# Kernel tuning notes

Hardware: AMD Instinct MI355X
Metric: run time of the kernel (lower is better)

Reference implementation:

```python
import jax, jax.numpy as jnp
import numpy as np

P = 2  # lrtd_pad (p_l == p_r == p_t == p_d)
B, C, H, W = 4, 64, 128, 128


def setup_inputs() -> dict:
    key = jax.random.key(0)
    x = jax.random.normal(key, (B, 6, C, H, W), dtype=jnp.float32)
    return {"x": x}


def _cube_pad(x):
    # faces: [B,C,H,W] each; order matches torch module unpacking
    fb, fd, ff, fl, fr, ft = (x[:, i] for i in range(6))
    flip_h = lambda a: a[:, :, ::-1, :]   # flip along dim 2 (rows)
    flip_w = lambda a: a[:, :, :, ::-1]   # flip along dim 3 (cols)
    T = lambda a: jnp.swapaxes(a, 2, 3)   # permute(0,1,3,2)

    # top strips for faces 0..5 -> [B,6,C,P,W]
    top = jnp.stack([
        flip_h(ft[:, :, :P, :]),           # back
        ff[:, :, -P:, :],                  # down
        ft[:, :, -P:, :],                  # front
        T(ft[:, :, :, :P]),                # left
        flip_h(T(ft[:, :, :, -P:])),       # right
        flip_h(fb[:, :, :P, :]),           # top
    ], axis=1)

    # bottom strips -> [B,6,C,P,W]
    bot = jnp.stack([
        flip_h(fd[:, :, -P:, :]),
        flip_h(fb[:, :, -P:, :]),
        fd[:, :, :P, :],
        flip_h(T(fd[:, :, :, :P])),
        T(fd[:, :, :, -P:]),
        ff[:, :, :P, :],
    ], axis=1)

    # left strips -> [B,6,C,H,P]
    lft = jnp.stack([
        fr[:, :, :, -P:],
        flip_w(T(fl[:, :, -P:, :])),
        fl[:, :, :, -P:],
        fb[:, :, :, -P:],
        ff[:, :, :, -P:],
        T(fl[:, :, :P, :]),
    ], axis=1)

    # right strips -> [B,6,C,H,P]
    rgt = jnp.stack([
        fl[:, :, :, :P],
        T(fr[:, :, -P:, :]),
        fr[:, :, :, :P],
        ff[:, :, :, :P],
        fb[:, :, :, :P],
        flip_w(T(fr[:, :, :P, :])),
    ], axis=1)

    # corners: equal pads -> repeat the top/bottom strip's edge column along width
    p_tl = jnp.tile(top[:, :, :, :P, :1], (1, 1, 1, 1, P))
    p_tr = jnp.tile(top[:, :, :, -P:, -1:], (1, 1, 1, 1, P))
    p_dl = jnp.tile(bot[:, :, :, :P, :1], (1, 1, 1, 1, P))
    p_dr = jnp.tile(bot[:, :, :, -P:, -1:], (1, 1, 1, 1, P))

    mid = jnp.concatenate([top, x, bot], axis=3)            # [B,6,C,H+2P,W]
    left = jnp.concatenate([p_tl, lft, p_dl], axis=3)       # [B,6,C,H+2P,P]
    right = jnp.concatenate([p_tr, rgt, p_dr], axis=3)      # [B,6,C,H+2P,P]
    return jnp.concatenate([left, mid, right], axis=4)      # [B,6,C,H+2P,W+2P]


def reference(x):
    return _cube_pad(x)
```

## Files before the change

### kernel.cpp

```cpp
#include <hip/hip_runtime.h>


constexpr int P = 2, B = 4, C = 64, H = 128, W = 128;
constexpr int Ho = H + 2 * P, Wo = W + 2 * P;
constexpr int NV = Wo / 4;
constexpr int TOTAL_V = B * 6 * C * Ho * NV;

__device__ __forceinline__ void top_map(int f, int t, int w, int& sf, int& r, int& col) {
    switch (f) {
        case 0:  sf = 5; r = P - 1 - t; col = w;         break;
        case 1:  sf = 2; r = H - P + t; col = w;         break;
        case 2:  sf = 5; r = H - P + t; col = w;         break;
        case 3:  sf = 5; r = w;         col = t;         break;
        case 4:  sf = 5; r = w;         col = W - 1 - t; break;
        default: sf = 0; r = P - 1 - t; col = w;         break;
    }
}
__device__ __forceinline__ void bot_map(int f, int t, int w, int& sf, int& r, int& col) {
    switch (f) {
        case 0:  sf = 1; r = H - 1 - t; col = w;         break;
        case 1:  sf = 0; r = H - 1 - t; col = w;         break;
        case 2:  sf = 1; r = t;         col = w;         break;
        case 3:  sf = 1; r = w;         col = P - 1 - t; break;
        case 4:  sf = 1; r = w;         col = W - P + t; break;
        default: sf = 2; r = t;         col = w;         break;
    }
}
__device__ __forceinline__ void lft_map(int f, int h, int l, int& sf, int& r, int& col) {
    switch (f) {
        case 0:  sf = 4; r = h;         col = W - P + l; break;
        case 1:  sf = 3; r = H - 1 - l; col = h;         break;
        case 2:  sf = 3; r = h;         col = W - P + l; break;
        case 3:  sf = 0; r = h;         col = W - P + l; break;
        case 4:  sf = 2; r = h;         col = W - P + l; break;
        default: sf = 3; r = l;         col = h;         break;
    }
}
__device__ __forceinline__ void rgt_map(int f, int h, int rr, int& sf, int& r, int& col) {
    switch (f) {
        case 0:  sf = 3; r = h;          col = rr;        break;
        case 1:  sf = 4; r = H - P + rr; col = h;         break;
        case 2:  sf = 4; r = h;          col = rr;        break;
        case 3:  sf = 2; r = h;          col = rr;        break;
        case 4:  sf = 0; r = h;          col = rr;        break;
        default: sf = 4; r = P - 1 - rr; col = h;         break;
    }
}

__device__ __forceinline__ void gen_map(int f, int i, int j, int& sf, int& r, int& col) {
    bool in_h = (i >= P) && (i < H + P);
    bool in_w = (j >= P) && (j < W + P);
    if (in_h && in_w) {
        sf = f; r = i - P; col = j - P;
    } else if (!in_h) {
        int w = in_w ? (j - P) : (j < P ? 0 : W - 1);
        if (i < P) top_map(f, i, w, sf, r, col);
        else       bot_map(f, i - H - P, w, sf, r, col);
    } else {
        if (j < P) lft_map(f, i - P, j,         sf, r, col);
        else       rgt_map(f, i - P, j - W - P, sf, r, col);
    }
}

__global__ __launch_bounds__(256) void cubepad_v4_kernel(const float* __restrict__ x,
                                                         float* __restrict__ out) {
    int idx = blockIdx.x * 256 + threadIdx.x;
    if (idx >= TOTAL_V) return;

    int v    = idx % NV;
    int t1   = idx / NV;
    int i    = t1 % Ho;
    int rest = t1 / Ho;
    int f    = (rest / C) % 6;
    int bC   = (rest / (C * 6)) * 6 * C + (rest % C);

    float4 val;
    float* vp = (float*)&val;
    size_t out_off = (size_t)t1 * Wo + 4 * v;

    bool fast = (i >= P) && (i < H + P) && (v >= 1) && (v < NV - 1);
    if (fast) {
        const float* src = x + ((size_t)(bC + f * C)) * (H * W)
                             + (size_t)(i - P) * W + (4 * v - P);
        float2 lo = *(const float2*)(src);
        float2 hi = *(const float2*)(src + 2);
        val = make_float4(lo.x, lo.y, hi.x, hi.y);
    } else {
        #pragma unroll
        for (int e = 0; e < 4; ++e) {
            int sf, r, col;
            gen_map(f, i, 4 * v + e, sf, r, col);
            vp[e] = x[((size_t)(bC + sf * C)) * (H * W) + (size_t)r * W + col];
        }
    }
    *(float4*)(out + out_off) = val;
}

extern "C" void kernel_launch(void* const* d_in, const int* in_sizes, int n_in,
                              void* d_out, int out_size, void* d_ws, size_t ws_size,
                              hipStream_t stream) {
    const float* x = (const float*)d_in[0];
    float* out = (float*)d_out;
    int blocks = (TOTAL_V + 255) / 256;
    cubepad_v4_kernel<<<blocks, 256, 0, stream>>>(x, out);
}
```

Before: 182.3 us.

## Split cube-pad into aligned interior row copy and separate halo blocks

Interior rows are now copied by 32-lane groups, each lane doing one aligned float4 load. A wavefront shuffle shifts the data by the pad width before an aligned float4 store. This replaces the two misaligned float2 loads per output vector and the per-element div/mod index math. Edge columns and top/bottom halo rows go to a separate set of blocks that keep the generic face-mapping gather. The halo work becomes a separate tail of smaller, divergent blocks, and correctness relies on lane 0 of each 32-group skipping its store.

```diff
diff --git a/kernel.cpp b/kernel.cpp
--- a/kernel.cpp
+++ b/kernel.cpp
@@ -4,7 +4,16 @@
 constexpr int P = 2, B = 4, C = 64, H = 128, W = 128;
 constexpr int Ho = H + 2 * P, Wo = W + 2 * P;
 constexpr int NV = Wo / 4;
-constexpr int TOTAL_V = B * 6 * C * Ho * NV;
+constexpr int PLANES = B * 6 * C;
+constexpr int ROWS   = PLANES * H;
+
+constexpr int NA   = ROWS * 32;
+constexpr int BLKA = NA / 256;
+
+constexpr int NMIX  = ROWS * 2;
+constexpr int NHALO = PLANES * 4 * NV;
+constexpr int NB    = NMIX + NHALO;
+constexpr int BLKB  = (NB + 255) / 256;
 
 __device__ __forceinline__ void top_map(int f, int t, int w, int& sf, int& r, int& col) {
     switch (f) {
@@ -62,38 +71,62 @@
     }
 }
 
-__global__ __launch_bounds__(256) void cubepad_v4_kernel(const float* __restrict__ x,
+__global__ __launch_bounds__(256) void cubepad_v5_kernel(const float* __restrict__ x,
                                                          float* __restrict__ out) {
-    int idx = blockIdx.x * 256 + threadIdx.x;
-    if (idx >= TOTAL_V) return;
+    const int bid = blockIdx.x;
+    const int tid = threadIdx.x;
 
-    int v    = idx % NV;
-    int t1   = idx / NV;
-    int i    = t1 % Ho;
-    int rest = t1 / Ho;
-    int f    = (rest / C) % 6;
-    int bC   = (rest / (C * 6)) * 6 * C + (rest % C);
+    if (bid < BLKA) {
+        const int idx = bid * 256 + tid;
+        const int g   = tid & 31;
+        const int row = idx >> 5;
+        const int i   = row & (H - 1);
+        const int p   = row >> 7;
+
+        const float4 v = *(const float4*)(x + ((size_t)row << 7) + (g << 2));
+
+        const float pz = __shfl_up(v.z, 1);
+        const float pw = __shfl_up(v.w, 1);
+
+        if (g != 0) {
+            const size_t o = (size_t)p * (Ho * Wo) + (size_t)(i + P) * Wo + (g << 2);
+            *(float4*)(out + o) = make_float4(pz, pw, v.x, v.y);
+        }
+        return;
+    }
+
+    const int m = (bid - BLKA) * 256 + tid;
+    if (m >= NB) return;
+
+    int p, i_out, v;
+    if (m < NMIX) {
+        const int row = m >> 1;
+        v     = (m & 1) ? (NV - 1) : 0;
+        i_out = (row & (H - 1)) + P;
+        p     = row >> 7;
+    } else {
+        const int h = m - NMIX;
+        const int g = h % NV;
+        const int t = (h / NV) & 3;
+        p     = h / (NV * 4);
+        v     = g;
+        i_out = (t < 2) ? t : (H + P + t - 2);
+    }
+
+    const int f  = (p / C) % 6;
+    const int b  = p / (6 * C);
+    const int bC = b * 6 * C + (p & (C - 1));
 
     float4 val;
     float* vp = (float*)&val;
-    size_t out_off = (size_t)t1 * Wo + 4 * v;
-
-    bool fast = (i >= P) && (i < H + P) && (v >= 1) && (v < NV - 1);
-    if (fast) {
-        const float* src = x + ((size_t)(bC + f * C)) * (H * W)
-                             + (size_t)(i - P) * W + (4 * v - P);
-        float2 lo = *(const float2*)(src);
-        float2 hi = *(const float2*)(src + 2);
-        val = make_float4(lo.x, lo.y, hi.x, hi.y);
-    } else {
-        #pragma unroll
-        for (int e = 0; e < 4; ++e) {
-            int sf, r, col;
-            gen_map(f, i, 4 * v + e, sf, r, col);
-            vp[e] = x[((size_t)(bC + sf * C)) * (H * W) + (size_t)r * W + col];
-        }
+    #pragma unroll
+    for (int e = 0; e < 4; ++e) {
+        int sf, r, col;
+        gen_map(f, i_out, 4 * v + e, sf, r, col);
+        vp[e] = x[((size_t)(bC + sf * C)) * (H * W) + ((size_t)r << 7) + col];
     }
-    *(float4*)(out + out_off) = val;
+    const size_t o = (size_t)p * (Ho * Wo) + (size_t)i_out * Wo + ((size_t)v << 2);
+    *(float4*)(out + o) = val;
 }
 
 extern "C" void kernel_launch(void* const* d_in, const int* in_sizes, int n_in,
@@ -101,6 +134,6 @@
                               hipStream_t stream) {
     const float* x = (const float*)d_in[0];
     float* out = (float*)d_out;
-    int blocks = (TOTAL_V + 255) / 256;
-    cubepad_v4_kernel<<<blocks, 256, 0, stream>>>(x, out);
+    const int blocks = BLKA + BLKB;
+    cubepad_v5_kernel<<<blocks, 256, 0, stream>>>(x, out);
 }
```

After: 210.5 us. 1.16x slower.

## Split cube-pad into aligned interior copy, edge-column, and halo-row block groups

Applied to the files above, without the earlier changes.

Restructures the work so most blocks copy interior rows with aligned 16-byte loads from the input and write them at a +2 offset with nontemporal stores. Separate block ranges handle the left/right 2-wide halo columns (one thread per row) and the top/bottom halo rows through the general face mapping. This replaces the old per-output-vector indexing, which read each interior vector as two misaligned float2 loads and had divergent fast/slow paths. The interior stores are only 8-byte aligned, which may split into narrower writes, and several block types now share one launch.

```diff
diff --git a/kernel.cpp b/kernel.cpp
--- a/kernel.cpp
+++ b/kernel.cpp
@@ -1,10 +1,21 @@
 #include <hip/hip_runtime.h>
 
+
+typedef float f32x4 __attribute__((ext_vector_type(4)));
+typedef f32x4 f32x4_a8 __attribute__((aligned(8)));
 
 constexpr int P = 2, B = 4, C = 64, H = 128, W = 128;
 constexpr int Ho = H + 2 * P, Wo = W + 2 * P;
 constexpr int NV = Wo / 4;
-constexpr int TOTAL_V = B * 6 * C * Ho * NV;
+constexpr int PLANES = B * 6 * C;
+constexpr int ROWS   = PLANES * H;
+
+constexpr int BLK_EDGE = ROWS / 256;
+constexpr int NHALO    = PLANES * 4 * NV;
+constexpr int BLK_HALO = NHALO / 256;
+constexpr int BLK_A    = ROWS * 32 / 256;
+constexpr int BLK_B    = BLK_EDGE + BLK_HALO;
+constexpr int BLOCKS   = BLK_B + BLK_A;
 
 __device__ __forceinline__ void top_map(int f, int t, int w, int& sf, int& r, int& col) {
     switch (f) {
@@ -62,38 +73,67 @@
     }
 }
 
-__global__ __launch_bounds__(256) void cubepad_v4_kernel(const float* __restrict__ x,
+__global__ __launch_bounds__(256) void cubepad_v8_kernel(const float* __restrict__ x,
                                                          float* __restrict__ out) {
-    int idx = blockIdx.x * 256 + threadIdx.x;
-    if (idx >= TOTAL_V) return;
+    const int bid = blockIdx.x;
+    const int tid = threadIdx.x;
 
-    int v    = idx % NV;
-    int t1   = idx / NV;
-    int i    = t1 % Ho;
-    int rest = t1 / Ho;
-    int f    = (rest / C) % 6;
-    int bC   = (rest / (C * 6)) * 6 * C + (rest % C);
+    if (bid >= BLK_B) {
+        const unsigned idx = (unsigned)(bid - BLK_B) * 256u + (unsigned)tid;
+        const unsigned g   = idx & 31u;
+        const unsigned row = idx >> 5;
+        const unsigned i   = row & (unsigned)(H - 1);
+        const unsigned p   = row >> 7;
 
-    float4 val;
-    float* vp = (float*)&val;
-    size_t out_off = (size_t)t1 * Wo + 4 * v;
+        const f32x4 v = *(const f32x4*)(x + ((size_t)row << 7) + (g << 2));
 
-    bool fast = (i >= P) && (i < H + P) && (v >= 1) && (v < NV - 1);
-    if (fast) {
-        const float* src = x + ((size_t)(bC + f * C)) * (H * W)
-                             + (size_t)(i - P) * W + (4 * v - P);
-        float2 lo = *(const float2*)(src);
-        float2 hi = *(const float2*)(src + 2);
-        val = make_float4(lo.x, lo.y, hi.x, hi.y);
-    } else {
-        #pragma unroll
-        for (int e = 0; e < 4; ++e) {
-            int sf, r, col;
-            gen_map(f, i, 4 * v + e, sf, r, col);
-            vp[e] = x[((size_t)(bC + sf * C)) * (H * W) + (size_t)r * W + col];
-        }
+        const size_t o = (size_t)p * (Ho * Wo) + (size_t)(i + P) * Wo + (g << 2) + P;
+        __builtin_nontemporal_store(v, (f32x4_a8*)(out + o));
+        return;
     }
-    *(float4*)(out + out_off) = val;
+
+    if (bid < BLK_EDGE) {
+        const unsigned row = (unsigned)bid * 256u + (unsigned)tid;
+        const unsigned i   = row & (unsigned)(H - 1);
+        const unsigned p   = row >> 7;
+        const int f  = (int)((p >> 6) % 6u);
+        const int bC = (int)(((p >> 6) / 6u) * (6u * C) + (p & 63u));
+
+        int sf, r, col;
+        float2 lv, rv;
+        lft_map(f, (int)i, 0, sf, r, col);
+        lv.x = x[((size_t)(bC + sf * C)) * (H * W) + ((size_t)r << 7) + col];
+        lft_map(f, (int)i, 1, sf, r, col);
+        lv.y = x[((size_t)(bC + sf * C)) * (H * W) + ((size_t)r << 7) + col];
+        rgt_map(f, (int)i, 0, sf, r, col);
+        rv.x = x[((size_t)(bC + sf * C)) * (H * W) + ((size_t)r << 7) + col];
+        rgt_map(f, (int)i, 1, sf, r, col);
+        rv.y = x[((size_t)(bC + sf * C)) * (H * W) + ((size_t)r << 7) + col];
+
+        const size_t rb = (size_t)p * (Ho * Wo) + (size_t)(i + P) * Wo;
+        *(float2*)(out + rb)            = lv;
+        *(float2*)(out + rb + (W + P))  = rv;
+        return;
+    }
+
+    const unsigned h = (unsigned)(bid - BLK_EDGE) * 256u + (unsigned)tid;
+    const unsigned v    = h % (unsigned)NV;
+    const unsigned t2   = h / (unsigned)NV;
+    const unsigned t    = t2 & 3u;
+    const unsigned p    = t2 >> 2;
+    const int i_out = (t < 2u) ? (int)t : (H + P + (int)t - 2);
+    const int f  = (int)((p >> 6) % 6u);
+    const int bC = (int)(((p >> 6) / 6u) * (6u * C) + (p & 63u));
+
+    f32x4 val;
+    #pragma unroll
+    for (int e = 0; e < 4; ++e) {
+        int sf, r, col;
+        gen_map(f, i_out, (int)(4u * v) + e, sf, r, col);
+        val[e] = x[((size_t)(bC + sf * C)) * (H * W) + ((size_t)r << 7) + col];
+    }
+    const size_t o = (size_t)p * (Ho * Wo) + (size_t)i_out * Wo + ((size_t)v << 2);
+    __builtin_nontemporal_store(val, (f32x4*)(out + o));
 }
 
 extern "C" void kernel_launch(void* const* d_in, const int* in_sizes, int n_in,
@@ -101,6 +141,5 @@
                               hipStream_t stream) {
     const float* x = (const float*)d_in[0];
     float* out = (float*)d_out;
-    int blocks = (TOTAL_V + 255) / 256;
-    cubepad_v4_kernel<<<blocks, 256, 0, stream>>>(x, out);
+    cubepad_v8_kernel<<<BLOCKS, 256, 0, stream>>>(x, out);
 }
```

New measurement: 193.2 us. 1.06x slower.
